# Optimization experiments

Hardware: AMD Instinct MI355X
Metric: run time of the kernel (lower is better)

## Reference

```python
import jax, jax.numpy as jnp
import numpy as np

N_NODES = 50000
N_EDGES = 800000


def setup_inputs() -> dict:
    key = jax.random.key(0)
    k1, k2, k3, k4, k5 = jax.random.split(key, 5)
    feat = jax.random.normal(k1, (N_NODES, 256), dtype=jnp.float32)
    src = jax.random.randint(k2, (N_EDGES,), 0, N_NODES, dtype=jnp.int32)
    dst = jax.random.randint(k3, (N_EDGES,), 0, N_NODES, dtype=jnp.int32)
    W1 = jax.random.normal(k4, (256, 128), dtype=jnp.float32) * (1.0 / np.sqrt(256))
    b1 = jnp.zeros((128,), dtype=jnp.float32)
    W2 = jax.random.normal(k5, (128, 32), dtype=jnp.float32) * (1.0 / np.sqrt(128))
    b2 = jnp.zeros((32,), dtype=jnp.float32)
    return {"feat": feat, "src": src, "dst": dst, "W1": W1, "b1": b1, "W2": W2, "b2": b2}


def _graph_conv(src, dst, x, W, b, n_nodes):
    # DGL GraphConv, norm='both': D_in^{-1/2} A D_out^{-1/2} X W + b
    ones = jnp.ones(src.shape, dtype=x.dtype)
    deg_out = jnp.clip(jax.ops.segment_sum(ones, src, num_segments=n_nodes), 1.0)
    deg_in = jnp.clip(jax.ops.segment_sum(ones, dst, num_segments=n_nodes), 1.0)
    h = x * (deg_out ** -0.5)[:, None]      # source-side normalization
    h = h @ W                                # project first (in_feats >= out_feats)
    m = jax.ops.segment_sum(h[src], dst, num_segments=n_nodes)  # SpMM aggregation
    return m * (deg_in ** -0.5)[:, None] + b


def reference(feat, src, dst, W1, b1, W2, b2):
    n_nodes = feat.shape[0]
    h = jax.nn.relu(_graph_conv(src, dst, feat, W1, b1, n_nodes))
    # dropout is identity in eval mode (training=False)
    h = _graph_conv(src, dst, h, W2, b2, n_nodes)
    return jax.nn.log_softmax(h, axis=1)
```

## Files before the change

### kernel.cpp

```cpp
#include <hip/hip_runtime.h>
#include <hip/hip_bf16.h>

#define N_NODES 50000
#define N_EDGES 800000
#define NB_SCAN 196
#define BH      64
#define EDG_B   12500
#define GRAN    3125
#define LDSW    25000

typedef __bf16 bf16_t;
typedef bf16_t bf16x8 __attribute__((ext_vector_type(8)));
typedef float  f32x4  __attribute__((ext_vector_type(4)));

static __device__ __forceinline__ float bfhi_to_f(uint v) {
    return __builtin_bit_cast(float, v & 0xffff0000u);
}
static __device__ __forceinline__ float bflo_to_f(uint v) {
    return __builtin_bit_cast(float, v << 16);
}
static __device__ __forceinline__ ushort f_to_bf(float x) {
    bf16_t q = (bf16_t)x;
    return __builtin_bit_cast(ushort, q);
}

__global__ __launch_bounds__(512) void histpack_kernel(const int* __restrict__ src,
                                                       const int* __restrict__ dst,
                                                       const float* __restrict__ W1,
                                                       const float* __restrict__ W2,
                                                       ushort* __restrict__ s16,
                                                       ushort* __restrict__ d16,
                                                       ushort* __restrict__ Pd,
                                                       ushort* __restrict__ Ps,
                                                       ushort* __restrict__ W1T,
                                                       ushort* __restrict__ W2T) {
    __shared__ uint h[LDSW];
    int bid = blockIdx.x;
    int tid = threadIdx.x;
    if (bid >= 2 * BH) {
        int t = (bid - 2 * BH) * 512 + tid;
        for (int i = t; i < 32768; i += 6 * 512) {
            int j = i >> 8, k = i & 255;
            W1T[i] = f_to_bf(W1[k * 128 + j]);
        }
        for (int i = t; i < 4096; i += 6 * 512) {
            int j = i >> 7, k = i & 127;
            W2T[i] = f_to_bf(W2[k * 32 + j]);
        }
        return;
    }
    for (int i = tid; i < LDSW; i += 512) h[i] = 0;
    __syncthreads();
    bool is_dst = bid < BH;
    int part = is_dst ? bid : bid - BH;
    const int4* iv = (const int4*)((is_dst ? dst : src) + part * EDG_B);
    ushort* ov = (is_dst ? d16 : s16) + part * EDG_B;
    for (int g = tid; g < GRAN; g += 512) {
        int4 v = iv[g];
        ushort4 p;
        p.x = (ushort)v.x; p.y = (ushort)v.y; p.z = (ushort)v.z; p.w = (ushort)v.w;
        *(ushort4*)(ov + g * 4) = p;
        atomicAdd(&h[v.x >> 1], 1u << ((v.x & 1) * 16));
        atomicAdd(&h[v.y >> 1], 1u << ((v.y & 1) * 16));
        atomicAdd(&h[v.z >> 1], 1u << ((v.z & 1) * 16));
        atomicAdd(&h[v.w >> 1], 1u << ((v.w & 1) * 16));
    }
    __syncthreads();
    uint* P = (uint*)((is_dst ? Pd : Ps) + part * N_NODES);
    for (int i = tid; i < LDSW; i += 512) P[i] = h[i];
}

__global__ __launch_bounds__(256) void scan1_kernel(const ushort* __restrict__ Pd,
                                                    const ushort* __restrict__ Ps,
                                                    int* __restrict__ deg_dst,
                                                    int* __restrict__ row_start,
                                                    int* __restrict__ blocksum,
                                                    float* __restrict__ dn_in,
                                                    float* __restrict__ dn_out) {
    __shared__ int s[256];
    int i = blockIdx.x * 256 + threadIdx.x;
    int v = 0;
    if (i < N_NODES) {
        int u = 0;
        for (int b = 0; b < BH; ++b) {
            v += Pd[b * N_NODES + i];
            u += Ps[b * N_NODES + i];
        }
        deg_dst[i] = v;
        dn_in[i]  = 1.0f / sqrtf(fmaxf((float)v, 1.0f));
        dn_out[i] = 1.0f / sqrtf(fmaxf((float)u, 1.0f));
    }
    s[threadIdx.x] = v;
    __syncthreads();
    for (int off = 1; off < 256; off <<= 1) {
        int t = (threadIdx.x >= off) ? s[threadIdx.x - off] : 0;
        __syncthreads();
        s[threadIdx.x] += t;
        __syncthreads();
    }
    if (i < N_NODES) row_start[i] = s[threadIdx.x] - v;
    if (threadIdx.x == 255) blocksum[blockIdx.x] = s[255];
}

__global__ __launch_bounds__(256) void scanfix_offs_kernel(const int* __restrict__ blocksum,
                                                           const ushort* __restrict__ Pd,
                                                           int* __restrict__ row_start,
                                                           uint* __restrict__ offs) {
    __shared__ int bs[256];
    int v = (threadIdx.x < NB_SCAN) ? blocksum[threadIdx.x] : 0;
    bs[threadIdx.x] = v;
    __syncthreads();
    for (int off = 1; off < 256; off <<= 1) {
        int t = (threadIdx.x >= off) ? bs[threadIdx.x - off] : 0;
        __syncthreads();
        bs[threadIdx.x] += t;
        __syncthreads();
    }
    int add = (blockIdx.x > 0) ? bs[blockIdx.x - 1] : 0;
    int i = blockIdx.x * 256 + threadIdx.x;
    if (i >= N_NODES) return;
    int acc = row_start[i] + add;
    row_start[i] = acc;
    for (int b = 0; b < BH; ++b) {
        offs[b * N_NODES + i] = (uint)acc;
        acc += Pd[b * N_NODES + i];
    }
}

__global__ __launch_bounds__(512) void fill_kernel(const ushort* __restrict__ d16,
                                                   const ushort* __restrict__ s16,
                                                   const uint* __restrict__ offs,
                                                   ushort* __restrict__ es16) {
    __shared__ uint lpos[LDSW];
    int tid = threadIdx.x, b = blockIdx.x;
    for (int i = tid; i < LDSW; i += 512) lpos[i] = 0;
    __syncthreads();
    const uint* of = offs + b * N_NODES;
    const ushort4* dv = (const ushort4*)(d16 + b * EDG_B);
    const ushort4* sv = (const ushort4*)(s16 + b * EDG_B);
#define FILL1(dd, ss) { int d_ = (int)(dd); uint sh_ = (uint)(d_ & 1) * 16; \
        uint old_ = atomicAdd(&lpos[d_ >> 1], 1u << sh_); \
        uint loc_ = (old_ >> sh_) & 0xffffu; \
        es16[of[d_] + loc_] = (ushort)(ss); }
    for (int g = tid; g < GRAN; g += 512) {
        ushort4 d4 = dv[g];
        ushort4 s4 = sv[g];
        FILL1(d4.x, s4.x);
        FILL1(d4.y, s4.y);
        FILL1(d4.z, s4.z);
        FILL1(d4.w, s4.w);
    }
#undef FILL1
}

__global__ __launch_bounds__(256) void gemm1_kernel(const float* __restrict__ feat,
                                                    const ushort* __restrict__ W1T,
                                                    const float* __restrict__ dn_out,
                                                    ushort* __restrict__ hp) {
    int wave = (blockIdx.x * 256 + threadIdx.x) >> 6;
    if (wave >= 3125) return;
    int lane = threadIdx.x & 63;
    int r0 = wave * 16;
    int row = r0 + (lane & 15);
    int ksel = (lane >> 4) * 8;
    float scale = dn_out[row];
    const float* fr = feat + row * 256 + ksel;
    const bf16x8* w1 = (const bf16x8*)W1T;

    f32x4 acc[8];
#pragma unroll
    for (int jt = 0; jt < 8; ++jt) acc[jt] = (f32x4){0.f, 0.f, 0.f, 0.f};

#pragma unroll
    for (int kc = 0; kc < 8; ++kc) {
        float4 f0 = *(const float4*)(fr + kc * 32);
        float4 f1 = *(const float4*)(fr + kc * 32 + 4);
        bf16x8 a;
        a[0] = (bf16_t)(f0.x * scale); a[1] = (bf16_t)(f0.y * scale);
        a[2] = (bf16_t)(f0.z * scale); a[3] = (bf16_t)(f0.w * scale);
        a[4] = (bf16_t)(f1.x * scale); a[5] = (bf16_t)(f1.y * scale);
        a[6] = (bf16_t)(f1.z * scale); a[7] = (bf16_t)(f1.w * scale);
        int kidx = (kc * 32 + ksel) >> 3;
#pragma unroll
        for (int jt = 0; jt < 8; ++jt) {
            int j = jt * 16 + (lane & 15);
            bf16x8 b = w1[j * 32 + kidx];
            acc[jt] = __builtin_amdgcn_mfma_f32_16x16x32_bf16(a, b, acc[jt], 0, 0, 0);
        }
    }
    int rbase = r0 + (lane >> 4) * 4;
#pragma unroll
    for (int jt = 0; jt < 8; ++jt) {
        int j = jt * 16 + (lane & 15);
#pragma unroll
        for (int r = 0; r < 4; ++r) {
            hp[(rbase + r) * 128 + j] = f_to_bf(acc[jt][r]);
        }
    }
}

__global__ __launch_bounds__(256) void agg1_kernel(const int* __restrict__ row_start,
                                                   const int* __restrict__ deg_dst,
                                                   const ushort* __restrict__ es16,
                                                   const ushort* __restrict__ hp,
                                                   const float* __restrict__ dn_in,
                                                   const float* __restrict__ dn_out,
                                                   const float* __restrict__ b1,
                                                   ushort* __restrict__ h1s) {
    int wid = threadIdx.x >> 6;
    int lane = threadIdx.x & 63;
    int n = blockIdx.x * 4 + wid;
    if (n >= N_NODES) return;
    int beg = row_start[n];
    int len = deg_dst[n];
    int c = lane * 2;
    const ushort* hb = hp + c;
    float ax = 0.f, ay = 0.f;
    int j = 0;
    for (; j + 7 < len; j += 8) {
        int i0 = es16[beg + j + 0], i1 = es16[beg + j + 1];
        int i2 = es16[beg + j + 2], i3 = es16[beg + j + 3];
        int i4 = es16[beg + j + 4], i5 = es16[beg + j + 5];
        int i6 = es16[beg + j + 6], i7 = es16[beg + j + 7];
        uint v0 = *(const uint*)(hb + i0 * 128);
        uint v1 = *(const uint*)(hb + i1 * 128);
        uint v2 = *(const uint*)(hb + i2 * 128);
        uint v3 = *(const uint*)(hb + i3 * 128);
        uint v4 = *(const uint*)(hb + i4 * 128);
        uint v5 = *(const uint*)(hb + i5 * 128);
        uint v6 = *(const uint*)(hb + i6 * 128);
        uint v7 = *(const uint*)(hb + i7 * 128);
        ax += ((bflo_to_f(v0) + bflo_to_f(v1)) + (bflo_to_f(v2) + bflo_to_f(v3)))
            + ((bflo_to_f(v4) + bflo_to_f(v5)) + (bflo_to_f(v6) + bflo_to_f(v7)));
        ay += ((bfhi_to_f(v0) + bfhi_to_f(v1)) + (bfhi_to_f(v2) + bfhi_to_f(v3)))
            + ((bfhi_to_f(v4) + bfhi_to_f(v5)) + (bfhi_to_f(v6) + bfhi_to_f(v7)));
    }
    for (; j + 1 < len; j += 2) {
        int i0 = es16[beg + j + 0], i1 = es16[beg + j + 1];
        uint v0 = *(const uint*)(hb + i0 * 128);
        uint v1 = *(const uint*)(hb + i1 * 128);
        ax += bflo_to_f(v0) + bflo_to_f(v1);
        ay += bfhi_to_f(v0) + bfhi_to_f(v1);
    }
    if (j < len) {
        uint v0 = *(const uint*)(hb + (int)es16[beg + j] * 128);
        ax += bflo_to_f(v0);
        ay += bfhi_to_f(v0);
    }
    float dn_i = dn_in[n], dn_o = dn_out[n];
    float x0 = fmaxf(ax * dn_i + b1[c], 0.f) * dn_o;
    float x1 = fmaxf(ay * dn_i + b1[c + 1], 0.f) * dn_o;
    uint pk = (uint)f_to_bf(x0) | ((uint)f_to_bf(x1) << 16);
    *(uint*)(h1s + n * 128 + c) = pk;
}

__global__ __launch_bounds__(256) void gemm2_kernel(const ushort* __restrict__ h1s,
                                                    const ushort* __restrict__ W2T,
                                                    ushort* __restrict__ hp2) {
    int wave = (blockIdx.x * 256 + threadIdx.x) >> 6;
    if (wave >= 3125) return;
    int lane = threadIdx.x & 63;
    int r0 = wave * 16;
    int row = r0 + (lane & 15);
    const bf16x8* av = (const bf16x8*)(h1s + row * 128);
    const bf16x8* w2 = (const bf16x8*)W2T;

    f32x4 acc[2];
    acc[0] = (f32x4){0.f, 0.f, 0.f, 0.f};
    acc[1] = (f32x4){0.f, 0.f, 0.f, 0.f};
#pragma unroll
    for (int kc = 0; kc < 4; ++kc) {
        bf16x8 a = av[kc * 4 + (lane >> 4)];
#pragma unroll
        for (int jt = 0; jt < 2; ++jt) {
            int j = jt * 16 + (lane & 15);
            bf16x8 b = w2[j * 16 + kc * 4 + (lane >> 4)];
            acc[jt] = __builtin_amdgcn_mfma_f32_16x16x32_bf16(a, b, acc[jt], 0, 0, 0);
        }
    }
    int rbase = r0 + (lane >> 4) * 4;
#pragma unroll
    for (int jt = 0; jt < 2; ++jt) {
        int j = jt * 16 + (lane & 15);
#pragma unroll
        for (int r = 0; r < 4; ++r) {
            hp2[(rbase + r) * 32 + j] = f_to_bf(acc[jt][r]);
        }
    }
}

__global__ __launch_bounds__(256) void agg2lsm_kernel(const int* __restrict__ row_start,
                                                      const int* __restrict__ deg_dst,
                                                      const ushort* __restrict__ es16,
                                                      const ushort* __restrict__ hp2,
                                                      const float* __restrict__ dn_in,
                                                      const float* __restrict__ b2,
                                                      float* __restrict__ out) {
    int g = threadIdx.x >> 5;
    int lane = threadIdx.x & 31;
    int n = blockIdx.x * 8 + g;
    if (n >= N_NODES) return;
    int beg = row_start[n];
    int len = deg_dst[n];
    const ushort* hb = hp2 + lane;
    float acc = 0.f;
    int j = 0;
    for (; j + 7 < len; j += 8) {
        int i0 = es16[beg + j + 0], i1 = es16[beg + j + 1];
        int i2 = es16[beg + j + 2], i3 = es16[beg + j + 3];
        int i4 = es16[beg + j + 4], i5 = es16[beg + j + 5];
        int i6 = es16[beg + j + 6], i7 = es16[beg + j + 7];
        float v0 = bflo_to_f((uint)hb[i0 * 32]);
        float v1 = bflo_to_f((uint)hb[i1 * 32]);
        float v2 = bflo_to_f((uint)hb[i2 * 32]);
        float v3 = bflo_to_f((uint)hb[i3 * 32]);
        float v4 = bflo_to_f((uint)hb[i4 * 32]);
        float v5 = bflo_to_f((uint)hb[i5 * 32]);
        float v6 = bflo_to_f((uint)hb[i6 * 32]);
        float v7 = bflo_to_f((uint)hb[i7 * 32]);
        acc += ((v0 + v1) + (v2 + v3)) + ((v4 + v5) + (v6 + v7));
    }
    for (; j + 1 < len; j += 2) {
        int i0 = es16[beg + j + 0], i1 = es16[beg + j + 1];
        acc += bflo_to_f((uint)hb[i0 * 32]) + bflo_to_f((uint)hb[i1 * 32]);
    }
    if (j < len) acc += bflo_to_f((uint)hb[(int)es16[beg + j] * 32]);
    float x = acc * dn_in[n] + b2[lane];
    float mx = x;
    for (int m = 16; m; m >>= 1) mx = fmaxf(mx, __shfl_xor(mx, m, 32));
    float ex = expf(x - mx);
    float s = ex;
    for (int m = 16; m; m >>= 1) s += __shfl_xor(s, m, 32);
    out[n * 32 + lane] = x - mx - logf(s);
}

extern "C" void kernel_launch(void* const* d_in, const int* in_sizes, int n_in,
                              void* d_out, int out_size, void* d_ws, size_t ws_size,
                              hipStream_t stream) {
    const float* feat = (const float*)d_in[0];
    const int*   src  = (const int*)d_in[1];
    const int*   dst  = (const int*)d_in[2];
    const float* W1   = (const float*)d_in[3];
    const float* b1   = (const float*)d_in[4];
    const float* W2   = (const float*)d_in[5];
    const float* b2   = (const float*)d_in[6];
    float* out = (float*)d_out;

    int*   iws       = (int*)d_ws;
    int*   deg_dst   = iws;
    int*   row_start = iws + 50000;
    int*   blocksum  = iws + 100000;
    ushort* Pd       = (ushort*)(iws + 100256);
    ushort* Ps       = (ushort*)(iws + 1700256);
    uint*  offs      = (uint*)(iws + 3300256);
    ushort* d16      = (ushort*)(iws + 6500256);
    ushort* s16      = (ushort*)(iws + 6900256);
    ushort* es16     = (ushort*)(iws + 7300256);
    float* fws       = (float*)d_ws;
    float* dn_out    = fws + 7700256;
    float* dn_in     = fws + 7750256;
    ushort* W1T = (ushort*)(fws + 7800256);
    ushort* W2T = (ushort*)(fws + 7816640);
    ushort* hp  = (ushort*)(fws + 7818688);
    ushort* h1s = (ushort*)(fws + 11018688);
    ushort* hp2 = (ushort*)(fws + 14218688);

    histpack_kernel<<<2 * BH + 6, 512, 0, stream>>>(src, dst, W1, W2,
                                                    s16, d16, Pd, Ps, W1T, W2T);
    scan1_kernel<<<NB_SCAN, 256, 0, stream>>>(Pd, Ps, deg_dst, row_start, blocksum,
                                              dn_in, dn_out);
    scanfix_offs_kernel<<<NB_SCAN, 256, 0, stream>>>(blocksum, Pd, row_start, offs);
    fill_kernel<<<BH, 512, 0, stream>>>(d16, s16, offs, es16);

    gemm1_kernel<<<(3125 * 64 + 255) / 256, 256, 0, stream>>>(feat, W1T, dn_out, hp);
    agg1_kernel<<<(N_NODES + 3) / 4, 256, 0, stream>>>(row_start, deg_dst, es16,
                                                       hp, dn_in, dn_out, b1, h1s);
    gemm2_kernel<<<(3125 * 64 + 255) / 256, 256, 0, stream>>>(h1s, W2T, hp2);
    agg2lsm_kernel<<<(N_NODES + 7) / 8, 256, 0, stream>>>(row_start, deg_dst, es16,
                                                          hp2, dn_in, b2, out);
}
```

Before: 249.9 us.

## Stage scaled feature tile in LDS and split GEMM1 output columns across waves

GEMM1 now assigns one 16-row tile per block instead of per wave. The block loads the tile with coalesced float4 reads, scales and converts it to bf16 once into LDS, and each of the 4 waves computes 32 of the 128 output columns. This is meant to give coalesced global reads of feat and spread the MFMA work over more waves for better latency hiding. In exchange it adds a barrier, an LDS round trip, and a 4x larger grid.

```diff
diff --git a/kernel.cpp b/kernel.cpp
--- a/kernel.cpp
+++ b/kernel.cpp
@@ -157,44 +157,47 @@
                                                     const ushort* __restrict__ W1T,
                                                     const float* __restrict__ dn_out,
                                                     ushort* __restrict__ hp) {
-    int wave = (blockIdx.x * 256 + threadIdx.x) >> 6;
-    if (wave >= 3125) return;
-    int lane = threadIdx.x & 63;
-    int r0 = wave * 16;
-    int row = r0 + (lane & 15);
-    int ksel = (lane >> 4) * 8;
-    float scale = dn_out[row];
-    const float* fr = feat + row * 256 + ksel;
+    __shared__ ushort a_lds[16][256 + 8];
+    int r0 = blockIdx.x * 16;
+    int tid = threadIdx.x;
+    for (int g = tid; g < 1024; g += 256) {
+        int row = g >> 6;
+        int c4 = (g & 63) * 4;
+        float4 f = *(const float4*)(feat + (r0 + row) * 256 + c4);
+        float sc = dn_out[r0 + row];
+        ushort4 q;
+        q.x = f_to_bf(f.x * sc); q.y = f_to_bf(f.y * sc);
+        q.z = f_to_bf(f.z * sc); q.w = f_to_bf(f.w * sc);
+        *(ushort4*)&a_lds[row][c4] = q;
+    }
+    __syncthreads();
+    int wid = tid >> 6;
+    int lane = tid & 63;
+    int l15 = lane & 15;
+    int khalf = lane >> 4;
     const bf16x8* w1 = (const bf16x8*)W1T;
-
-    f32x4 acc[8];
-#pragma unroll
-    for (int jt = 0; jt < 8; ++jt) acc[jt] = (f32x4){0.f, 0.f, 0.f, 0.f};
-
+    f32x4 acc[2];
+    acc[0] = (f32x4){0.f, 0.f, 0.f, 0.f};
+    acc[1] = (f32x4){0.f, 0.f, 0.f, 0.f};
+    int jt0 = wid * 2;
 #pragma unroll
     for (int kc = 0; kc < 8; ++kc) {
-        float4 f0 = *(const float4*)(fr + kc * 32);
-        float4 f1 = *(const float4*)(fr + kc * 32 + 4);
-        bf16x8 a;
-        a[0] = (bf16_t)(f0.x * scale); a[1] = (bf16_t)(f0.y * scale);
-        a[2] = (bf16_t)(f0.z * scale); a[3] = (bf16_t)(f0.w * scale);
-        a[4] = (bf16_t)(f1.x * scale); a[5] = (bf16_t)(f1.y * scale);
-        a[6] = (bf16_t)(f1.z * scale); a[7] = (bf16_t)(f1.w * scale);
-        int kidx = (kc * 32 + ksel) >> 3;
-#pragma unroll
-        for (int jt = 0; jt < 8; ++jt) {
-            int j = jt * 16 + (lane & 15);
+        bf16x8 a = *(const bf16x8*)&a_lds[l15][kc * 32 + khalf * 8];
+        int kidx = kc * 4 + khalf;
+#pragma unroll
+        for (int q = 0; q < 2; ++q) {
+            int j = (jt0 + q) * 16 + l15;
             bf16x8 b = w1[j * 32 + kidx];
-            acc[jt] = __builtin_amdgcn_mfma_f32_16x16x32_bf16(a, b, acc[jt], 0, 0, 0);
-        }
-    }
-    int rbase = r0 + (lane >> 4) * 4;
-#pragma unroll
-    for (int jt = 0; jt < 8; ++jt) {
-        int j = jt * 16 + (lane & 15);
+            acc[q] = __builtin_amdgcn_mfma_f32_16x16x32_bf16(a, b, acc[q], 0, 0, 0);
+        }
+    }
+    int rbase = r0 + khalf * 4;
+#pragma unroll
+    for (int q = 0; q < 2; ++q) {
+        int j = (jt0 + q) * 16 + l15;
 #pragma unroll
         for (int r = 0; r < 4; ++r) {
-            hp[(rbase + r) * 128 + j] = f_to_bf(acc[jt][r]);
+            hp[(rbase + r) * 128 + j] = f_to_bf(acc[q][r]);
         }
     }
 }
@@ -372,7 +375,7 @@
     scanfix_offs_kernel<<<NB_SCAN, 256, 0, stream>>>(blocksum, Pd, row_start, offs);
     fill_kernel<<<BH, 512, 0, stream>>>(d16, s16, offs, es16);
 
-    gemm1_kernel<<<(3125 * 64 + 255) / 256, 256, 0, stream>>>(feat, W1T, dn_out, hp);
+    gemm1_kernel<<<3125, 256, 0, stream>>>(feat, W1T, dn_out, hp);
     agg1_kernel<<<(N_NODES + 3) / 4, 256, 0, stream>>>(row_start, deg_dst, es16,
                                                        hp, dn_in, dn_out, b1, h1s);
     gemm2_kernel<<<(3125 * 64 + 255) / 256, 256, 0, stream>>>(h1s, W2T, hp2);
```

Result: faster. 241.6 us (-3.3%).
